# Kernel optimization log

Measured on AMD Instinct MI355X. Metric: run time of the kernel, lower is better.

The kernel has to match this reference:

```python
import jax, jax.numpy as jnp
import numpy as np
from jax import lax

T, B, I, H, O = 2048, 512, 5, 64, 1


def _lstm_layer(x_seq, W_ih, W_hh, b_ih, b_hh):
    """Single LSTM layer, PyTorch gate order (i, f, g, o).
    x_seq: [T, B, in], returns all hidden states [T, B, H]."""
    Hd = W_hh.shape[1]
    Bd = x_seq.shape[1]
    # Precompute input projections for all timesteps in one big GEMM.
    x_proj = jnp.einsum('tbi,gi->tbg', x_seq, W_ih) + b_ih + b_hh  # [T,B,4H]

    def step(carry, xp_t):
        h, c = carry
        gates = xp_t + h @ W_hh.T  # [B, 4H]
        i, f, g, o = jnp.split(gates, 4, axis=-1)
        i = jax.nn.sigmoid(i)
        f = jax.nn.sigmoid(f)
        g = jnp.tanh(g)
        o = jax.nn.sigmoid(o)
        c = f * c + i * g
        h = o * jnp.tanh(c)
        return (h, c), h

    h0 = jnp.zeros((Bd, Hd), dtype=x_seq.dtype)
    c0 = jnp.zeros((Bd, Hd), dtype=x_seq.dtype)
    _, hs = lax.scan(step, (h0, c0), x_proj)
    return hs


def setup_inputs() -> dict:
    key = jax.random.key(0)
    ks = jax.random.split(key, 11)
    s = 1.0 / np.sqrt(H)  # PyTorch LSTM default init scale
    inp = {
        'x': jax.random.normal(ks[0], (T, B, I), dtype=jnp.float32),
        'W_ih0': jax.random.uniform(ks[1], (4 * H, I), jnp.float32, -s, s),
        'W_hh0': jax.random.uniform(ks[2], (4 * H, H), jnp.float32, -s, s),
        'b_ih0': jax.random.uniform(ks[3], (4 * H,), jnp.float32, -s, s),
        'b_hh0': jax.random.uniform(ks[4], (4 * H,), jnp.float32, -s, s),
        'W_ih1': jax.random.uniform(ks[5], (4 * H, H), jnp.float32, -s, s),
        'W_hh1': jax.random.uniform(ks[6], (4 * H, H), jnp.float32, -s, s),
        'b_ih1': jax.random.uniform(ks[7], (4 * H,), jnp.float32, -s, s),
        'b_hh1': jax.random.uniform(ks[8], (4 * H,), jnp.float32, -s, s),
        # self.out: Linear(H, 1), weight ~ N(0, 1/0.01) per init_weights
        'W_out': jax.random.normal(ks[9], (O, H), dtype=jnp.float32) * (1.0 / 0.01),
        'b_out': jax.random.uniform(ks[10], (O,), jnp.float32, -s, s),
    }
    return inp


def reference(x, W_ih0, W_hh0, b_ih0, b_hh0, W_ih1, W_hh1, b_ih1, b_hh1, W_out, b_out):
    h1 = _lstm_layer(x, W_ih0, W_hh0, b_ih0, b_hh0)     # [T,B,H]
    h2 = _lstm_layer(h1, W_ih1, W_hh1, b_ih1, b_hh1)    # [T,B,H]
    # out(r_out[-1, :, :]) -> [B, 1]
    return h2[-1] @ W_out.T + b_out
```

## Files before the change

kernel.cpp:

```cpp
#include <hip/hip_runtime.h>

#define TT 2048
#define BB 512
#define II 5
#define HH 64

__device__ __forceinline__ float sigm(float v)   { return 1.0f / (1.0f + __expf(-v)); }
__device__ __forceinline__ float tanh_f(float v) { return 1.0f - 2.0f / (1.0f + __expf(2.0f * v)); }

__global__ __launch_bounds__(256, 2) void lstm2_kernel(
    const float* __restrict__ x,
    const float* __restrict__ W_ih0, const float* __restrict__ W_hh0,
    const float* __restrict__ b_ih0, const float* __restrict__ b_hh0,
    const float* __restrict__ W_ih1, const float* __restrict__ W_hh1,
    const float* __restrict__ b_ih1, const float* __restrict__ b_hh1,
    const float* __restrict__ W_out, const float* __restrict__ b_out,
    float* __restrict__ out)
{
    const int t = threadIdx.x;
    const int b = blockIdx.x;
    const int gate = t >> 6;

    __shared__ __align__(16) float act[256];
    __shared__ __align__(16) float h1s[HH];
    __shared__ __align__(16) float h2s[HH];

    float wih0[II];
    #pragma unroll
    for (int k = 0; k < II; ++k) wih0[k] = W_ih0[t * II + k];
    const float bias0 = b_ih0[t] + b_hh0[t];
    const float bias1 = b_ih1[t] + b_hh1[t];

    float4 whh0[16], wih1[16], whh1[16];
    const float4* p0 = (const float4*)(W_hh0 + t * HH);
    const float4* p1 = (const float4*)(W_ih1 + t * HH);
    const float4* p2 = (const float4*)(W_hh1 + t * HH);
    #pragma unroll
    for (int k = 0; k < 16; ++k) { whh0[k] = p0[k]; wih1[k] = p1[k]; whh1[k] = p2[k]; }

    float c1 = 0.0f, c2 = 0.0f;
    if (t < HH) { h1s[t] = 0.0f; h2s[t] = 0.0f; }
    __syncthreads();

    const float* xb = x + b * II;
    float xc[II];
    #pragma unroll
    for (int k = 0; k < II; ++k) xc[k] = xb[k];

    for (int step = 0; step < TT; ++step) {
        float xn[II];
        if (step + 1 < TT) {
            const float* xnp = xb + (size_t)(step + 1) * (BB * II);
            #pragma unroll
            for (int k = 0; k < II; ++k) xn[k] = xnp[k];
        }

        float acc = bias0;
        #pragma unroll
        for (int k = 0; k < II; ++k) acc = fmaf(xc[k], wih0[k], acc);
        #pragma unroll
        for (int k = 0; k < 16; ++k) {
            float4 h = ((const float4*)h1s)[k];
            acc = fmaf(h.x, whh0[k].x, acc);
            acc = fmaf(h.y, whh0[k].y, acc);
            acc = fmaf(h.z, whh0[k].z, acc);
            acc = fmaf(h.w, whh0[k].w, acc);
        }
        act[t] = (gate == 2) ? tanh_f(acc) : sigm(acc);
        __syncthreads();

        if (t < HH) {
            float iv = act[t], fv = act[HH + t], gv = act[2 * HH + t], ov = act[3 * HH + t];
            c1 = fv * c1 + iv * gv;
            h1s[t] = ov * tanh_f(c1);
        }
        __syncthreads();

        float acc2 = bias1;
        #pragma unroll
        for (int k = 0; k < 16; ++k) {
            float4 h = ((const float4*)h1s)[k];
            acc2 = fmaf(h.x, wih1[k].x, acc2);
            acc2 = fmaf(h.y, wih1[k].y, acc2);
            acc2 = fmaf(h.z, wih1[k].z, acc2);
            acc2 = fmaf(h.w, wih1[k].w, acc2);
        }
        #pragma unroll
        for (int k = 0; k < 16; ++k) {
            float4 h = ((const float4*)h2s)[k];
            acc2 = fmaf(h.x, whh1[k].x, acc2);
            acc2 = fmaf(h.y, whh1[k].y, acc2);
            acc2 = fmaf(h.z, whh1[k].z, acc2);
            acc2 = fmaf(h.w, whh1[k].w, acc2);
        }
        act[t] = (gate == 2) ? tanh_f(acc2) : sigm(acc2);
        __syncthreads();

        if (t < HH) {
            float iv = act[t], fv = act[HH + t], gv = act[2 * HH + t], ov = act[3 * HH + t];
            c2 = fv * c2 + iv * gv;
            h2s[t] = ov * tanh_f(c2);
        }
        __syncthreads();

        #pragma unroll
        for (int k = 0; k < II; ++k) xc[k] = xn[k];
    }

    if (t < HH) {
        float v = h2s[t] * W_out[t];
        #pragma unroll
        for (int off = 32; off > 0; off >>= 1) v += __shfl_xor(v, off);
        if (t == 0) out[b] = v + b_out[0];
    }
}

extern "C" void kernel_launch(void* const* d_in, const int* in_sizes, int n_in,
                              void* d_out, int out_size, void* d_ws, size_t ws_size,
                              hipStream_t stream) {
    const float* x     = (const float*)d_in[0];
    const float* W_ih0 = (const float*)d_in[1];
    const float* W_hh0 = (const float*)d_in[2];
    const float* b_ih0 = (const float*)d_in[3];
    const float* b_hh0 = (const float*)d_in[4];
    const float* W_ih1 = (const float*)d_in[5];
    const float* W_hh1 = (const float*)d_in[6];
    const float* b_ih1 = (const float*)d_in[7];
    const float* b_hh1 = (const float*)d_in[8];
    const float* W_out = (const float*)d_in[9];
    const float* b_out = (const float*)d_in[10];
    float* out = (float*)d_out;

    lstm2_kernel<<<dim3(BB), dim3(256), 0, stream>>>(
        x, W_ih0, W_hh0, b_ih0, b_hh0, W_ih1, W_hh1, b_ih1, b_hh1, W_out, b_out, out);
}
```

Before: 3.160 ms.

## Wavefront-pipeline the two LSTM layers across thread groups, two batch rows per block

The kernel now uses 768 threads split into three groups, each holding one weight matrix (W_hh0, W_ih1, W_hh1). Layer 1 at step s runs concurrently with layer 2 at step s-1, which halves the barriers per timestep from four to two. Each block processes two batch elements so every weight register is reused twice per shared-memory pass, and the input projection for the next step is computed ahead of time. The cost is more shared-memory buffers, larger blocks, one extra pipeline-drain iteration, and only 256 blocks, which may leave some compute units idle.

```diff
diff --git a/kernel.cpp b/kernel.cpp
--- a/kernel.cpp
+++ b/kernel.cpp
@@ -4,11 +4,12 @@
 #define BB 512
 #define II 5
 #define HH 64
+#define NTHR 768
 
 __device__ __forceinline__ float sigm(float v)   { return 1.0f / (1.0f + __expf(-v)); }
 __device__ __forceinline__ float tanh_f(float v) { return 1.0f - 2.0f / (1.0f + __expf(2.0f * v)); }
 
-__global__ __launch_bounds__(256, 2) void lstm2_kernel(
+__global__ __launch_bounds__(NTHR, 3) void lstm2_kernel(
     const float* __restrict__ x,
     const float* __restrict__ W_ih0, const float* __restrict__ W_hh0,
     const float* __restrict__ b_ih0, const float* __restrict__ b_hh0,
@@ -17,101 +18,129 @@
     const float* __restrict__ W_out, const float* __restrict__ b_out,
     float* __restrict__ out)
 {
-    const int t = threadIdx.x;
-    const int b = blockIdx.x;
-    const int gate = t >> 6;
+    const int tid = threadIdx.x;
+    const int g   = tid >> 8;
+    const int r   = tid & 255;
+    const int blk = blockIdx.x;
 
-    __shared__ __align__(16) float act[256];
-    __shared__ __align__(16) float h1s[HH];
-    __shared__ __align__(16) float h2s[HH];
+    __shared__ __align__(16) float h1s[2][HH];
+    __shared__ __align__(16) float h2s[2][HH];
+    __shared__ __align__(16) float act0[2][256];
+    __shared__ __align__(16) float pB[2][256];
+    __shared__ __align__(16) float pC[2][256];
+
+    const float* Wrow = (g == 0) ? (W_hh0 + r * HH)
+                      : (g == 1) ? (W_ih1 + r * HH)
+                                 : (W_hh1 + r * HH);
+    float4 w[16];
+    #pragma unroll
+    for (int k = 0; k < 16; ++k) w[k] = ((const float4*)Wrow)[k];
 
     float wih0[II];
-    #pragma unroll
-    for (int k = 0; k < II; ++k) wih0[k] = W_ih0[t * II + k];
-    const float bias0 = b_ih0[t] + b_hh0[t];
-    const float bias1 = b_ih1[t] + b_hh1[t];
-
-    float4 whh0[16], wih1[16], whh1[16];
-    const float4* p0 = (const float4*)(W_hh0 + t * HH);
-    const float4* p1 = (const float4*)(W_ih1 + t * HH);
-    const float4* p2 = (const float4*)(W_hh1 + t * HH);
-    #pragma unroll
-    for (int k = 0; k < 16; ++k) { whh0[k] = p0[k]; wih1[k] = p1[k]; whh1[k] = p2[k]; }
+    float bias0 = 0.0f, bias1 = 0.0f;
+    if (g == 0) {
+        #pragma unroll
+        for (int k = 0; k < II; ++k) wih0[k] = W_ih0[r * II + k];
+        bias0 = b_ih0[r] + b_hh0[r];
+    } else if (g == 1) {
+        bias1 = b_ih1[r] + b_hh1[r];
+    }
 
     float c1 = 0.0f, c2 = 0.0f;
-    if (t < HH) { h1s[t] = 0.0f; h2s[t] = 0.0f; }
+    if (tid < 2 * HH) { ((float*)h1s)[tid] = 0.0f; ((float*)h2s)[tid] = 0.0f; }
+
+    const float* xb0 = x + (size_t)(2 * blk + 0) * II;
+    const float* xb1 = x + (size_t)(2 * blk + 1) * II;
+
+    float xd0 = 0.0f, xd1 = 0.0f;
+    if (g == 0) {
+        #pragma unroll
+        for (int k = 0; k < II; ++k) {
+            xd0 = fmaf(xb0[k], wih0[k], xd0);
+            xd1 = fmaf(xb1[k], wih0[k], xd1);
+        }
+    }
     __syncthreads();
 
-    const float* xb = x + b * II;
-    float xc[II];
-    #pragma unroll
-    for (int k = 0; k < II; ++k) xc[k] = xb[k];
+    const int gate = r >> 6;
 
-    for (int step = 0; step < TT; ++step) {
-        float xn[II];
-        if (step + 1 < TT) {
-            const float* xnp = xb + (size_t)(step + 1) * (BB * II);
+    for (int s = 0; s <= TT; ++s) {
+        float xl0[II], xl1[II];
+        if (g == 0) {
+            const int sn = (s + 1 < TT) ? (s + 1) : (TT - 1);
+            const float* p0 = xb0 + (size_t)sn * (BB * II);
+            const float* p1 = xb1 + (size_t)sn * (BB * II);
             #pragma unroll
-            for (int k = 0; k < II; ++k) xn[k] = xnp[k];
+            for (int k = 0; k < II; ++k) { xl0[k] = p0[k]; xl1[k] = p1[k]; }
         }
 
-        float acc = bias0;
+        const float4* hp0 = (g == 2) ? (const float4*)h2s[0] : (const float4*)h1s[0];
+        const float4* hp1 = (g == 2) ? (const float4*)h2s[1] : (const float4*)h1s[1];
+        float d0a = 0.0f, d0b = 0.0f, d1a = 0.0f, d1b = 0.0f;
         #pragma unroll
-        for (int k = 0; k < II; ++k) acc = fmaf(xc[k], wih0[k], acc);
-        #pragma unroll
-        for (int k = 0; k < 16; ++k) {
-            float4 h = ((const float4*)h1s)[k];
-            acc = fmaf(h.x, whh0[k].x, acc);
-            acc = fmaf(h.y, whh0[k].y, acc);
-            acc = fmaf(h.z, whh0[k].z, acc);
-            acc = fmaf(h.w, whh0[k].w, acc);
+        for (int k = 0; k < 8; ++k) {
+            float4 he0 = hp0[2 * k], ho0 = hp0[2 * k + 1];
+            float4 he1 = hp1[2 * k], ho1 = hp1[2 * k + 1];
+            d0a = fmaf(he0.x, w[2*k].x, d0a);   d0b = fmaf(ho0.x, w[2*k+1].x, d0b);
+            d0a = fmaf(he0.y, w[2*k].y, d0a);   d0b = fmaf(ho0.y, w[2*k+1].y, d0b);
+            d0a = fmaf(he0.z, w[2*k].z, d0a);   d0b = fmaf(ho0.z, w[2*k+1].z, d0b);
+            d0a = fmaf(he0.w, w[2*k].w, d0a);   d0b = fmaf(ho0.w, w[2*k+1].w, d0b);
+            d1a = fmaf(he1.x, w[2*k].x, d1a);   d1b = fmaf(ho1.x, w[2*k+1].x, d1b);
+            d1a = fmaf(he1.y, w[2*k].y, d1a);   d1b = fmaf(ho1.y, w[2*k+1].y, d1b);
+            d1a = fmaf(he1.z, w[2*k].z, d1a);   d1b = fmaf(ho1.z, w[2*k+1].z, d1b);
+            d1a = fmaf(he1.w, w[2*k].w, d1a);   d1b = fmaf(ho1.w, w[2*k+1].w, d1b);
         }
-        act[t] = (gate == 2) ? tanh_f(acc) : sigm(acc);
-        __syncthreads();
+        float d0 = d0a + d0b, d1 = d1a + d1b;
 
-        if (t < HH) {
-            float iv = act[t], fv = act[HH + t], gv = act[2 * HH + t], ov = act[3 * HH + t];
-            c1 = fv * c1 + iv * gv;
-            h1s[t] = ov * tanh_f(c1);
+        if (g == 0) {
+            d0 += bias0 + xd0;
+            d1 += bias0 + xd1;
+            act0[0][r] = (gate == 2) ? tanh_f(d0) : sigm(d0);
+            act0[1][r] = (gate == 2) ? tanh_f(d1) : sigm(d1);
+            float a0 = 0.0f, a1 = 0.0f;
+            #pragma unroll
+            for (int k = 0; k < II; ++k) {
+                a0 = fmaf(xl0[k], wih0[k], a0);
+                a1 = fmaf(xl1[k], wih0[k], a1);
+            }
+            xd0 = a0; xd1 = a1;
+        } else if (g == 1) {
+            pB[0][r] = d0 + bias1;
+            pB[1][r] = d1 + bias1;
+        } else {
+            pC[0][r] = d0;
+            pC[1][r] = d1;
         }
         __syncthreads();
 
-        float acc2 = bias1;
-        #pragma unroll
-        for (int k = 0; k < 16; ++k) {
-            float4 h = ((const float4*)h1s)[k];
-            acc2 = fmaf(h.x, wih1[k].x, acc2);
-            acc2 = fmaf(h.y, wih1[k].y, acc2);
-            acc2 = fmaf(h.z, wih1[k].z, acc2);
-            acc2 = fmaf(h.w, wih1[k].w, acc2);
-        }
-        #pragma unroll
-        for (int k = 0; k < 16; ++k) {
-            float4 h = ((const float4*)h2s)[k];
-            acc2 = fmaf(h.x, whh1[k].x, acc2);
-            acc2 = fmaf(h.y, whh1[k].y, acc2);
-            acc2 = fmaf(h.z, whh1[k].z, acc2);
-            acc2 = fmaf(h.w, whh1[k].w, acc2);
-        }
-        act[t] = (gate == 2) ? tanh_f(acc2) : sigm(acc2);
-        __syncthreads();
-
-        if (t < HH) {
-            float iv = act[t], fv = act[HH + t], gv = act[2 * HH + t], ov = act[3 * HH + t];
-            c2 = fv * c2 + iv * gv;
-            h2s[t] = ov * tanh_f(c2);
+        if (g == 0) {
+            const int e = (tid >> 6) & 1;
+            const int l = tid & 63;
+            if (s < TT) {
+                float iv = act0[e][l],        fv = act0[e][64 + l];
+                float gv = act0[e][128 + l],  ov = act0[e][192 + l];
+                c1 = fmaf(fv, c1, iv * gv);
+                h1s[e][l] = ov * tanh_f(c1);
+            }
+            if (s >= 1) {
+                float bi = pB[e][l]       + pC[e][l];
+                float bf = pB[e][64 + l]  + pC[e][64 + l];
+                float bg = pB[e][128 + l] + pC[e][128 + l];
+                float bo = pB[e][192 + l] + pC[e][192 + l];
+                float iv = sigm(bi), fv = sigm(bf), gv = tanh_f(bg), ov = sigm(bo);
+                c2 = fmaf(fv, c2, iv * gv);
+                h2s[e][l] = ov * tanh_f(c2);
+            }
         }
         __syncthreads();
-
-        #pragma unroll
-        for (int k = 0; k < II; ++k) xc[k] = xn[k];
     }
 
-    if (t < HH) {
-        float v = h2s[t] * W_out[t];
+    if (tid < 2 * HH) {
+        const int e = tid >> 6, l = tid & 63;
+        float v = h2s[e][l] * W_out[l];
         #pragma unroll
         for (int off = 32; off > 0; off >>= 1) v += __shfl_xor(v, off);
-        if (t == 0) out[b] = v + b_out[0];
+        if (l == 0) out[2 * blk + e] = v + b_out[0];
     }
 }
 
@@ -131,6 +160,6 @@
     const float* b_out = (const float*)d_in[10];
     float* out = (float*)d_out;
 
-    lstm2_kernel<<<dim3(BB), dim3(256), 0, stream>>>(
+    lstm2_kernel<<<dim3(BB / 2), dim3(NTHR), 0, stream>>>(
         x, W_ih0, W_hh0, b_ih0, b_hh0, W_ih1, W_hh1, b_ih1, b_hh1, W_out, b_out, out);
 }
```

Result: slower. 9.450 ms (+199.0%).

## Pipeline both LSTM layers per step with split-K, two batch elements per block

Applied to the files above, without the earlier changes.

Restructures the recurrence so each 1024-thread block handles two batch elements. Each gate row's 64-wide dot product is split across four threads, with partial sums reduced through shared memory. Layer 1 at step s and layer 2 at step s-1 run in the same iteration, which cuts the barriers per timestep from four to two and shortens the serial critical path. The cost is a 256-block grid (about one block per CU), extra shared-memory traffic for partial-sum reduction, and one additional pipeline iteration.

```diff
diff --git a/kernel.cpp b/kernel.cpp
--- a/kernel.cpp
+++ b/kernel.cpp
@@ -3,12 +3,19 @@
 #define TT 2048
 #define BB 512
 #define II 5
-#define HH 64
 
 __device__ __forceinline__ float sigm(float v)   { return 1.0f / (1.0f + __expf(-v)); }
 __device__ __forceinline__ float tanh_f(float v) { return 1.0f - 2.0f / (1.0f + __expf(2.0f * v)); }
 
-__global__ __launch_bounds__(256, 2) void lstm2_kernel(
+__device__ __forceinline__ float dot4(float4 w, float4 h, float acc) {
+    acc = fmaf(h.x, w.x, acc);
+    acc = fmaf(h.y, w.y, acc);
+    acc = fmaf(h.z, w.z, acc);
+    acc = fmaf(h.w, w.w, acc);
+    return acc;
+}
+
+__global__ __launch_bounds__(1024) void lstm2_kernel(
     const float* __restrict__ x,
     const float* __restrict__ W_ih0, const float* __restrict__ W_hh0,
     const float* __restrict__ b_ih0, const float* __restrict__ b_hh0,
@@ -17,101 +24,130 @@
     const float* __restrict__ W_out, const float* __restrict__ b_out,
     float* __restrict__ out)
 {
-    const int t = threadIdx.x;
-    const int b = blockIdx.x;
-    const int gate = t >> 6;
+    const int t   = threadIdx.x;
+    const int blk = blockIdx.x;
+    const int q   = t >> 8;
+    const int r   = t & 255;
 
-    __shared__ __align__(16) float act[256];
-    __shared__ __align__(16) float h1s[HH];
-    __shared__ __align__(16) float h2s[HH];
+    __shared__ __align__(16) float big[21504];
+    float* pA  = big;
+    float* pD  = big + 2048;
+    float* h1s = big + 4096;
+    float* h2s = big + 4224;
+    float* xst = big + 4352;
 
-    float wih0[II];
-    #pragma unroll
-    for (int k = 0; k < II; ++k) wih0[k] = W_ih0[t * II + k];
-    const float bias0 = b_ih0[t] + b_hh0[t];
-    const float bias1 = b_ih1[t] + b_hh1[t];
+    float4 wA[4], wB[4], wC[4];
+    {
+        const float4* ap = (const float4*)(W_hh0 + r * 64 + q * 16);
+        const float4* bp = (const float4*)(W_ih1 + r * 64 + q * 16);
+        const float4* cp = (const float4*)(W_hh1 + r * 64 + q * 16);
+        #pragma unroll
+        for (int k = 0; k < 4; ++k) { wA[k] = ap[k]; wB[k] = bp[k]; wC[k] = cp[k]; }
+    }
+    float wih0[II], bias0 = 0.f, bias1 = 0.f;
+    if (q == 0) {
+        #pragma unroll
+        for (int k = 0; k < II; ++k) wih0[k] = W_ih0[r * II + k];
+        bias0 = b_ih0[r] + b_hh0[r];
+        bias1 = b_ih1[r] + b_hh1[r];
+    }
 
-    float4 whh0[16], wih1[16], whh1[16];
-    const float4* p0 = (const float4*)(W_hh0 + t * HH);
-    const float4* p1 = (const float4*)(W_ih1 + t * HH);
-    const float4* p2 = (const float4*)(W_hh1 + t * HH);
-    #pragma unroll
-    for (int k = 0; k < 16; ++k) { whh0[k] = p0[k]; wih1[k] = p1[k]; whh1[k] = p2[k]; }
+    if (t < 256) big[4096 + t] = 0.f;
+    if (t < 16) {
+        const int e = t >> 3, k = t & 7;
+        xst[t] = (k < II) ? x[(size_t)(2 * blk + e) * II + k] : 0.f;
+    }
 
-    float c1 = 0.0f, c2 = 0.0f;
-    if (t < HH) { h1s[t] = 0.0f; h2s[t] = 0.0f; }
+    float c = 0.f;
+    const int uw_e     = (t >> 7) & 1;
+    const int uw_layer = (t >> 6) & 1;
+    const int ul       = t & 63;
+
     __syncthreads();
 
-    const float* xb = x + b * II;
-    float xc[II];
-    #pragma unroll
-    for (int k = 0; k < II; ++k) xc[k] = xb[k];
-
-    for (int step = 0; step < TT; ++step) {
-        float xn[II];
-        if (step + 1 < TT) {
-            const float* xnp = xb + (size_t)(step + 1) * (BB * II);
-            #pragma unroll
-            for (int k = 0; k < II; ++k) xn[k] = xnp[k];
+    for (int s = 0; s <= TT; ++s) {
+        float xn = 0.f;
+        if (t < 16) {
+            const int sn = (s + 1 < TT) ? (s + 1) : (TT - 1);
+            const int e = t >> 3, k = t & 7;
+            if (k < II) xn = x[((size_t)sn * BB + 2 * blk + e) * II + k];
         }
 
-        float acc = bias0;
+        const float4* h1p0 = (const float4*)(h1s)      + q * 4;
+        const float4* h2p0 = (const float4*)(h2s)      + q * 4;
+        float accA0 = 0.f, accB0 = 0.f, accC0 = 0.f;
         #pragma unroll
-        for (int k = 0; k < II; ++k) acc = fmaf(xc[k], wih0[k], acc);
+        for (int k = 0; k < 4; ++k) {
+            float4 hv = h1p0[k];
+            accA0 = dot4(wA[k], hv, accA0);
+            accB0 = dot4(wB[k], hv, accB0);
+        }
         #pragma unroll
-        for (int k = 0; k < 16; ++k) {
-            float4 h = ((const float4*)h1s)[k];
-            acc = fmaf(h.x, whh0[k].x, acc);
-            acc = fmaf(h.y, whh0[k].y, acc);
-            acc = fmaf(h.z, whh0[k].z, acc);
-            acc = fmaf(h.w, whh0[k].w, acc);
+        for (int k = 0; k < 4; ++k) {
+            float4 hv = h2p0[k];
+            accC0 = dot4(wC[k], hv, accC0);
         }
-        act[t] = (gate == 2) ? tanh_f(acc) : sigm(acc);
+        __builtin_amdgcn_sched_barrier(0);
+        const float4* h1p1 = (const float4*)(h1s + 64) + q * 4;
+        const float4* h2p1 = (const float4*)(h2s + 64) + q * 4;
+        float accA1 = 0.f, accB1 = 0.f, accC1 = 0.f;
+        #pragma unroll
+        for (int k = 0; k < 4; ++k) {
+            float4 hv = h1p1[k];
+            accA1 = dot4(wA[k], hv, accA1);
+            accB1 = dot4(wB[k], hv, accB1);
+        }
+        #pragma unroll
+        for (int k = 0; k < 4; ++k) {
+            float4 hv = h2p1[k];
+            accC1 = dot4(wC[k], hv, accC1);
+        }
+
+        float d0 = accB0 + accC0;
+        float d1 = accB1 + accC1;
+        if (q == 0) {
+            const float* xs = xst + (s & 1) * 16;
+            float xd0 = 0.f, xd1 = 0.f;
+            #pragma unroll
+            for (int k = 0; k < II; ++k) {
+                xd0 = fmaf(xs[k],     wih0[k], xd0);
+                xd1 = fmaf(xs[8 + k], wih0[k], xd1);
+            }
+            accA0 += bias0 + xd0;
+            accA1 += bias0 + xd1;
+            d0 += bias1;
+            d1 += bias1;
+        }
+        pA[q * 256 + r]        = accA0;
+        pA[1024 + q * 256 + r] = accA1;
+        pD[q * 256 + r]        = d0;
+        pD[1024 + q * 256 + r] = d1;
+
+        if (t < 16) xst[((s + 1) & 1) * 16 + t] = xn;
         __syncthreads();
 
-        if (t < HH) {
-            float iv = act[t], fv = act[HH + t], gv = act[2 * HH + t], ov = act[3 * HH + t];
-            c1 = fv * c1 + iv * gv;
-            h1s[t] = ov * tanh_f(c1);
+        if (t < 256) {
+            const bool go = uw_layer ? (s >= 1) : (s < TT);
+            if (go) {
+                const float* P = (uw_layer ? pD : pA) + uw_e * 1024;
+                float pi = P[ul]       + P[256 + ul] + P[512 + ul] + P[768 + ul];
+                float pf = P[64 + ul]  + P[320 + ul] + P[576 + ul] + P[832 + ul];
+                float pg = P[128 + ul] + P[384 + ul] + P[640 + ul] + P[896 + ul];
+                float po = P[192 + ul] + P[448 + ul] + P[704 + ul] + P[960 + ul];
+                float iv = sigm(pi), fv = sigm(pf), gv = tanh_f(pg), ov = sigm(po);
+                c = fmaf(fv, c, iv * gv);
+                (uw_layer ? h2s : h1s)[uw_e * 64 + ul] = ov * tanh_f(c);
+            }
         }
         __syncthreads();
-
-        float acc2 = bias1;
-        #pragma unroll
-        for (int k = 0; k < 16; ++k) {
-            float4 h = ((const float4*)h1s)[k];
-            acc2 = fmaf(h.x, wih1[k].x, acc2);
-            acc2 = fmaf(h.y, wih1[k].y, acc2);
-            acc2 = fmaf(h.z, wih1[k].z, acc2);
-            acc2 = fmaf(h.w, wih1[k].w, acc2);
-        }
-        #pragma unroll
-        for (int k = 0; k < 16; ++k) {
-            float4 h = ((const float4*)h2s)[k];
-            acc2 = fmaf(h.x, whh1[k].x, acc2);
-            acc2 = fmaf(h.y, whh1[k].y, acc2);
-            acc2 = fmaf(h.z, whh1[k].z, acc2);
-            acc2 = fmaf(h.w, whh1[k].w, acc2);
-        }
-        act[t] = (gate == 2) ? tanh_f(acc2) : sigm(acc2);
-        __syncthreads();
-
-        if (t < HH) {
-            float iv = act[t], fv = act[HH + t], gv = act[2 * HH + t], ov = act[3 * HH + t];
-            c2 = fv * c2 + iv * gv;
-            h2s[t] = ov * tanh_f(c2);
-        }
-        __syncthreads();
-
-        #pragma unroll
-        for (int k = 0; k < II; ++k) xc[k] = xn[k];
     }
 
-    if (t < HH) {
-        float v = h2s[t] * W_out[t];
+    if (t < 128) {
+        const int e = t >> 6, l = t & 63;
+        float v = h2s[e * 64 + l] * W_out[l];
         #pragma unroll
         for (int off = 32; off > 0; off >>= 1) v += __shfl_xor(v, off);
-        if (t == 0) out[b] = v + b_out[0];
+        if (l == 0) out[2 * blk + e] = v + b_out[0];
     }
 }
 
@@ -131,6 +167,6 @@
     const float* b_out = (const float*)d_in[10];
     float* out = (float*)d_out;
 
-    lstm2_kernel<<<dim3(BB), dim3(256), 0, stream>>>(
+    lstm2_kernel<<<dim3(BB / 2), dim3(1024), 0, stream>>>(
         x, W_ih0, W_hh0, b_ih0, b_hh0, W_ih1, W_hh1, b_ih1, b_hh1, W_out, b_out, out);
 }
```

Result: slower. 11.22 ms (+255.0%).
